# Kernel tuning notes

Hardware: AMD Instinct MI355X
Metric: run time of the kernel (lower is better)

Reference implementation:

```python
import jax, jax.numpy as jnp
import numpy as np

E = 8          # num_experts
K = 2          # top_k
CAPF = 1.25    # capacity_factor
DIM = 512
HID = 2048     # int(dim * mlp_ratio)


def setup_inputs() -> dict:
    key = jax.random.key(0)
    ks = jax.random.split(key, 5)
    s = 0.02
    x = jax.random.normal(ks[0], (8, 2048, DIM), jnp.float32)
    Wr = jax.random.normal(ks[1], (E, DIM), jnp.float32) * s          # router weight (no bias)
    W1 = jax.random.normal(ks[2], (E, HID, DIM), jnp.float32) * s     # fc1 weights per expert
    b1 = jnp.zeros((E, HID), jnp.float32)
    W2 = jax.random.normal(ks[3], (E, DIM, HID), jnp.float32) * s     # fc2 weights per expert
    b2 = jnp.zeros((E, DIM), jnp.float32)
    return {"x": x, "Wr": Wr, "W1": W1, "b1": b1, "W2": W2, "b2": b2}


def _capacity_keep(top_w, top_idx, cap):
    """For each (slot, expert), keep only the `cap` highest-weight tokens.
    top_w, top_idx: [T, K]. Returns bool keep mask [T, K]."""
    def per_slot(w, idx):
        order = jnp.argsort(-w)                       # tokens sorted by weight desc
        idx_sorted = idx[order]                       # [T] expert id in sorted order
        oh = jax.nn.one_hot(idx_sorted, E, dtype=jnp.int32)
        rank = jnp.cumsum(oh, axis=0) - 1             # rank within each expert
        r = jnp.take_along_axis(rank, idx_sorted[:, None], axis=1)[:, 0]
        keep_sorted = r < cap
        return jnp.zeros(w.shape[0], bool).at[order].set(keep_sorted)
    return jax.vmap(per_slot, in_axes=(1, 1), out_axes=1)(top_w, top_idx)


def reference(x, Wr, W1, b1, W2, b2):
    b, n, d = x.shape
    T = b * n
    flat = x.reshape(T, d)

    # Router: softmax in fp32 then cast back
    logits = flat @ Wr.T                                            # [T, E]
    probs = jax.nn.softmax(logits.astype(jnp.float32), axis=-1).astype(flat.dtype)
    top_w, top_idx = jax.lax.top_k(probs, K)                        # [T, K]
    top_w = top_w / (jnp.sum(top_w, axis=-1, keepdims=True) + 1e-8)

    # Capacity-limited drop, then renormalize
    cap = max(1, int(CAPF * T * K / E))
    keep = _capacity_keep(top_w, top_idx, cap)
    top_w = jnp.where(keep, top_w, 0.0)
    top_w = top_w / jnp.clip(jnp.sum(top_w, axis=-1, keepdims=True), 1e-8, None)

    # Combine weight per (token, expert): scatter-add top_w into dense [T, E]
    rows = jnp.arange(T)[:, None]
    w_te = jnp.zeros((T, E), flat.dtype).at[rows, top_idx].add(top_w)

    # Per-expert MLP, weighted combine (w_te is 0 for unassigned/dropped pairs)
    out = jnp.zeros_like(flat)
    for e in range(E):
        h = jax.nn.gelu(flat @ W1[e].T + b1[e], approximate=False)  # [T, HID]
        y = h @ W2[e].T + b2[e]                                     # [T, D]
        out = out + w_te[:, e:e + 1] * y

    # Load-balancing aux loss
    load = jnp.sum(w_te, axis=0) / T
    importance = probs.mean(0)
    aux = jnp.sum(importance * load * float(E))
    return out.reshape(b, n, d), aux
```

## Files before the change

### kernel.cpp

```cpp
#include <hip/hip_runtime.h>
#include <hip/hip_bf16.h>
#include <math.h>

#define DIM 512
#define HID 2048
#define NE  8
#define CSTRIDE 32

typedef __attribute__((ext_vector_type(8))) short short8;
typedef __attribute__((ext_vector_type(4))) float f32x4;
typedef unsigned short ushort_t;

static __device__ __forceinline__ ushort_t f2bf(float f) {
    unsigned int x = __builtin_bit_cast(unsigned int, f);
    unsigned int lsb = (x >> 16) & 1u;
    x += 0x7fffu + lsb;
    return (ushort_t)(x >> 16);
}
static __device__ __forceinline__ float bf2f(ushort_t u) {
    unsigned int x = ((unsigned int)u) << 16;
    return __builtin_bit_cast(float, x);
}

static __device__ __forceinline__ float fast_gelu(float v) {
    float u = v * 0.70710678118654752f;
    float s = fabsf(u);
    float t = __builtin_amdgcn_rcpf(1.f + 0.3275911f * s);
    float poly = ((((1.061405429f * t - 1.453152027f) * t + 1.421413741f) * t
                   - 0.284496736f) * t + 0.254829592f) * t;
    float e = __expf(-s * s);
    float erfv = copysignf(1.f - poly * e, u);
    return 0.5f * v * (1.f + erfv);
}

static __device__ __forceinline__ void gld16(const void* g, void* l) {
    __builtin_amdgcn_global_load_lds(
        (const __attribute__((address_space(1))) void*)g,
        (__attribute__((address_space(3))) void*)l,
        16, 0, 0);
}

__global__ void k_cvt(const float* __restrict__ src, ushort_t* __restrict__ dst, int n) {
    int i = blockIdx.x * blockDim.x + threadIdx.x;
    int stride = gridDim.x * blockDim.x;
    int n4 = n >> 2;
    for (int j = i; j < n4; j += stride) {
        float4 v = ((const float4*)src)[j];
        ushort4 o;
        o.x = f2bf(v.x); o.y = f2bf(v.y); o.z = f2bf(v.z); o.w = f2bf(v.w);
        ((ushort4*)dst)[j] = o;
    }
}

__global__ __launch_bounds__(256) void k_router(const float* __restrict__ x,
    const float* __restrict__ Wr, ushort_t* __restrict__ xb,
    float* __restrict__ probs, int* __restrict__ tidx, float* __restrict__ tw, int T)
{
    int lane = threadIdx.x & 63;
    int t = blockIdx.x * 4 + (threadIdx.x >> 6);
    if (t >= T) return;
    const float* xr = x + (size_t)t * DIM;
    double acc[NE];
#pragma unroll
    for (int e = 0; e < NE; e++) acc[e] = 0.0;
    for (int i = lane; i < DIM; i += 64) {
        float xv = xr[i];
        xb[(size_t)t * DIM + i] = f2bf(xv);
        double xd = (double)xv;
#pragma unroll
        for (int e = 0; e < NE; e++) acc[e] += xd * (double)Wr[e * DIM + i];
    }
#pragma unroll
    for (int e = 0; e < NE; e++) {
#pragma unroll
        for (int off = 32; off > 0; off >>= 1) acc[e] += __shfl_xor(acc[e], off);
    }
    double mx = acc[0];
#pragma unroll
    for (int e = 1; e < NE; e++) mx = fmax(mx, acc[e]);
    double p[NE], sum = 0.0;
#pragma unroll
    for (int e = 0; e < NE; e++) { p[e] = exp(acc[e] - mx); sum += p[e]; }
    float pr[NE];
#pragma unroll
    for (int e = 0; e < NE; e++) pr[e] = (float)(p[e] / sum);
    if (lane < NE) probs[(size_t)t * NE + lane] = pr[lane];
    if (lane == 0) {
        int i1 = 0; float b1v = pr[0];
#pragma unroll
        for (int e = 1; e < NE; e++) if (pr[e] > b1v) { b1v = pr[e]; i1 = e; }
        int i2 = -1; float b2v = -1.f;
#pragma unroll
        for (int e = 0; e < NE; e++) if (e != i1 && pr[e] > b2v) { b2v = pr[e]; i2 = e; }
        float s2 = b1v + b2v + 1e-8f;
        tidx[t * 2] = i1; tidx[t * 2 + 1] = i2;
        tw[t * 2] = b1v / s2; tw[t * 2 + 1] = b2v / s2;
    }
}

__global__ __launch_bounds__(256) void k_hist(const int* __restrict__ tidx,
                                              int* __restrict__ cnt, int T) {
    __shared__ int h[16];
    if (threadIdx.x < 16) h[threadIdx.x] = 0;
    __syncthreads();
    int stride = gridDim.x * blockDim.x;
    for (int t = blockIdx.x * blockDim.x + threadIdx.x; t < T; t += stride) {
        atomicAdd(&h[tidx[t * 2]], 1);
        atomicAdd(&h[8 + tidx[t * 2 + 1]], 1);
    }
    __syncthreads();
    if (threadIdx.x < 16 && h[threadIdx.x] != 0)
        atomicAdd(&cnt[threadIdx.x * CSTRIDE], h[threadIdx.x]);
}

__global__ void k_keep(const int* __restrict__ tidx, const float* __restrict__ tw,
                       const int* __restrict__ cnt, float* __restrict__ tw2, int T, int cap)
{
    int t = blockIdx.x * blockDim.x + threadIdx.x;
    if (t >= T) return;
    float wk[2];
#pragma unroll
    for (int s = 0; s < 2; s++) {
        int e = tidx[t * 2 + s];
        float w = tw[t * 2 + s];
        wk[s] = w;
        if (cnt[(s * NE + e) * CSTRIDE] > cap) {
            int rank = 0;
            for (int t2 = 0; t2 < T; t2++) {
                if (tidx[t2 * 2 + s] == e) {
                    float w2 = tw[t2 * 2 + s];
                    if (w2 > w || (w2 == w && t2 < t)) rank++;
                }
            }
            if (rank >= cap) wk[s] = 0.f;
        }
    }
    float denom = fmaxf(wk[0] + wk[1], 1e-8f);
    tw2[t * 2]     = wk[0] / denom;
    tw2[t * 2 + 1] = wk[1] / denom;
}

__global__ __launch_bounds__(256) void k_build(const int* __restrict__ tidx,
        const float* __restrict__ tw2, int* __restrict__ lcnt,
        int* __restrict__ ltok, int* __restrict__ pos, int T, int capM)
{
    __shared__ int h[NE];
    __shared__ int base[NE];
    if (threadIdx.x < NE) h[threadIdx.x] = 0;
    __syncthreads();
    int t = blockIdx.x * blockDim.x + threadIdx.x;
    int myE[2] = {-1, -1};
    int myp[2] = {0, 0};
    if (t < T) {
#pragma unroll
        for (int s = 0; s < 2; s++) {
            float w = tw2[t * 2 + s];
            if (w != 0.f) {
                int e = tidx[t * 2 + s];
                myE[s] = e;
                myp[s] = atomicAdd(&h[e], 1);
            }
        }
    }
    __syncthreads();
    if (threadIdx.x < NE)
        base[threadIdx.x] = (h[threadIdx.x] != 0)
            ? atomicAdd(&lcnt[threadIdx.x * CSTRIDE], h[threadIdx.x]) : 0;
    __syncthreads();
    if (t < T) {
#pragma unroll
        for (int s = 0; s < 2; s++) {
            if (myE[s] >= 0) {
                int p = base[myE[s]] + myp[s];
                ltok[myE[s] * capM + p] = t;
                pos[t * 2 + s] = (myE[s] << 20) | p;
            } else {
                pos[t * 2 + s] = -1;
            }
        }
    }
}

__global__ void k_off(const int* __restrict__ lcnt, int* __restrict__ loff) {
    if (threadIdx.x == 0 && blockIdx.x == 0) {
        int o = 0;
        for (int e = 0; e < NE; e++) {
            loff[e] = o;
            o += ((lcnt[e * CSTRIDE] + 127) >> 7) << 7;
        }
        loff[NE] = o;
    }
}

__global__ __launch_bounds__(256) void k_fc1(
    const ushort_t* __restrict__ xb, const ushort_t* __restrict__ W1b,
    const float* __restrict__ b1, const int* __restrict__ lcnt,
    const int* __restrict__ loff, const int* __restrict__ ltok,
    ushort_t* __restrict__ hbuf, int capM)
{
    int bx = blockIdx.x;
    int e  = bx & 7;
    int r  = bx >> 3;
    int mt = r >> 4;
    int nt = r & 15;
    int cnt = lcnt[e * CSTRIDE];
    if (cnt > capM) cnt = capM;
    int m0 = mt * 128;
    if (m0 >= cnt) return;
    int n0 = nt * 128;
    const int* toks = ltok + e * capM;
    int hrow0 = loff[e] + m0;
    const ushort_t* Bsrc = W1b + (size_t)e * HID * DIM;

    __shared__ char smem[65536];
    char* As0 = smem;          char* Bs0 = smem + 16384;
    char* As1 = smem + 32768;  char* Bs1 = smem + 49152;

    int tid = threadIdx.x;
    int wave = tid >> 6, lane = tid & 63;
    int wm = wave >> 1, wn = wave & 1;

    const char* aSrc[4]; const char* bSrc[4]; int ldst[4];
#pragma unroll
    for (int i = 0; i < 4; i++) {
        int c = tid + 256 * i;
        int row = c >> 3, cc = c & 7;
        int scc = cc ^ (row & 7);
        int gr = m0 + row;
        int tok = toks[gr < cnt ? gr : (cnt - 1)];
        aSrc[i] = (const char*)(xb + (size_t)tok * DIM + scc * 8);
        bSrc[i] = (const char*)(Bsrc + (size_t)(n0 + row) * DIM + scc * 8);
        ldst[i] = (i * 256 + wave * 64) * 16;
    }

    f32x4 acc[4][4];
#pragma unroll
    for (int a = 0; a < 4; a++)
#pragma unroll
        for (int b = 0; b < 4; b++) acc[a][b] = (f32x4){0.f, 0.f, 0.f, 0.f};

    int aRow = wm * 64 + (lane & 15);
    int bRow = wn * 64 + (lane & 15);
    int kq = lane >> 4;

    auto STAGE = [&](int kt, char* A, char* B) {
#pragma unroll
        for (int i = 0; i < 4; i++) {
            gld16(aSrc[i] + kt * 128, A + ldst[i]);
            gld16(bSrc[i] + kt * 128, B + ldst[i]);
        }
    };
    auto COMPUTE = [&](const char* A, const char* B) {
#pragma unroll
        for (int kk = 0; kk < 2; kk++) {
            int c16 = kk * 4 + kq;
            short8 af[4], bfr[4];
#pragma unroll
            for (int mf = 0; mf < 4; mf++) {
                int rr = aRow + mf * 16;
                af[mf] = *(const short8*)(A + rr * 128 + ((c16 ^ (rr & 7)) << 4));
            }
#pragma unroll
            for (int nf = 0; nf < 4; nf++) {
                int rr = bRow + nf * 16;
                bfr[nf] = *(const short8*)(B + rr * 128 + ((c16 ^ (rr & 7)) << 4));
            }
#pragma unroll
            for (int mf = 0; mf < 4; mf++)
#pragma unroll
                for (int nf = 0; nf < 4; nf++)
                    acc[mf][nf] = __builtin_amdgcn_mfma_f32_16x16x32_bf16(bfr[nf], af[mf], acc[mf][nf], 0, 0, 0);
        }
    };

    const int NT = DIM / 64;
    char *Ac = As0, *Bc = Bs0, *An = As1, *Bn = Bs1;
    STAGE(0, Ac, Bc);
    __syncthreads();
    for (int kt = 0; kt < NT; kt++) {
        if (kt + 1 < NT) STAGE(kt + 1, An, Bn);
        COMPUTE(Ac, Bc);
        __syncthreads();
        char* t0 = Ac; Ac = An; An = t0;
        char* t1 = Bc; Bc = Bn; Bn = t1;
    }

    const float* b1e = b1 + e * HID;
    int mlocal = wm * 64 + (lane & 15);
    int nbase0 = n0 + wn * 64 + (lane >> 4) * 4;
#pragma unroll
    for (int mf = 0; mf < 4; mf++) {
        int mrow = mlocal + mf * 16;
        bool valid = (m0 + mrow) < cnt;
        ushort_t* dst = hbuf + (size_t)(hrow0 + mrow) * HID;
#pragma unroll
        for (int nf = 0; nf < 4; nf++) {
            int nc = nbase0 + nf * 16;
            float4 bias4 = *(const float4*)(b1e + nc);
            ushort4 o;
            o.x = f2bf(fast_gelu(acc[mf][nf][0] + bias4.x));
            o.y = f2bf(fast_gelu(acc[mf][nf][1] + bias4.y));
            o.z = f2bf(fast_gelu(acc[mf][nf][2] + bias4.z));
            o.w = f2bf(fast_gelu(acc[mf][nf][3] + bias4.w));
            if (valid) *(ushort4*)(dst + nc) = o;
        }
    }
}

__global__ __launch_bounds__(256) void k_fc2(
    const ushort_t* __restrict__ hbuf, const ushort_t* __restrict__ W2b,
    const float* __restrict__ b2, const int* __restrict__ lcnt,
    const int* __restrict__ loff, ushort_t* __restrict__ ybuf, int capM)
{
    int bx = blockIdx.x;
    int e  = bx & 7;
    int r  = bx >> 3;
    int mt = r >> 2;
    int nt = r & 3;
    int cnt = lcnt[e * CSTRIDE];
    if (cnt > capM) cnt = capM;
    int m0 = mt * 128;
    if (m0 >= cnt) return;
    int n0 = nt * 128;
    int hrow0 = loff[e] + m0;
    const ushort_t* Bsrc = W2b + (size_t)e * DIM * HID;

    __shared__ char smem[65536];
    char* As0 = smem;          char* Bs0 = smem + 16384;
    char* As1 = smem + 32768;  char* Bs1 = smem + 49152;

    int tid = threadIdx.x;
    int wave = tid >> 6, lane = tid & 63;
    int wm = wave >> 1, wn = wave & 1;

    const char* aSrc[4]; const char* bSrc[4]; int ldst[4];
#pragma unroll
    for (int i = 0; i < 4; i++) {
        int c = tid + 256 * i;
        int row = c >> 3, cc = c & 7;
        int scc = cc ^ (row & 7);
        aSrc[i] = (const char*)(hbuf + (size_t)(hrow0 + row) * HID + scc * 8);
        bSrc[i] = (const char*)(Bsrc + (size_t)(n0 + row) * HID + scc * 8);
        ldst[i] = (i * 256 + wave * 64) * 16;
    }

    f32x4 acc[4][4];
#pragma unroll
    for (int a = 0; a < 4; a++)
#pragma unroll
        for (int b = 0; b < 4; b++) acc[a][b] = (f32x4){0.f, 0.f, 0.f, 0.f};

    int aRow = wm * 64 + (lane & 15);
    int bRow = wn * 64 + (lane & 15);
    int kq = lane >> 4;

    auto STAGE = [&](int kt, char* A, char* B) {
#pragma unroll
        for (int i = 0; i < 4; i++) {
            gld16(aSrc[i] + kt * 128, A + ldst[i]);
            gld16(bSrc[i] + kt * 128, B + ldst[i]);
        }
    };
    auto COMPUTE = [&](const char* A, const char* B) {
#pragma unroll
        for (int kk = 0; kk < 2; kk++) {
            int c16 = kk * 4 + kq;
            short8 af[4], bfr[4];
#pragma unroll
            for (int mf = 0; mf < 4; mf++) {
                int rr = aRow + mf * 16;
                af[mf] = *(const short8*)(A + rr * 128 + ((c16 ^ (rr & 7)) << 4));
            }
#pragma unroll
            for (int nf = 0; nf < 4; nf++) {
                int rr = bRow + nf * 16;
                bfr[nf] = *(const short8*)(B + rr * 128 + ((c16 ^ (rr & 7)) << 4));
            }
#pragma unroll
            for (int mf = 0; mf < 4; mf++)
#pragma unroll
                for (int nf = 0; nf < 4; nf++)
                    acc[mf][nf] = __builtin_amdgcn_mfma_f32_16x16x32_bf16(bfr[nf], af[mf], acc[mf][nf], 0, 0, 0);
        }
    };

    const int NT = HID / 64;
    char *Ac = As0, *Bc = Bs0, *An = As1, *Bn = Bs1;
    STAGE(0, Ac, Bc);
    __syncthreads();
    for (int kt = 0; kt < NT; kt++) {
        if (kt + 1 < NT) STAGE(kt + 1, An, Bn);
        COMPUTE(Ac, Bc);
        __syncthreads();
        char* t0 = Ac; Ac = An; An = t0;
        char* t1 = Bc; Bc = Bn; Bn = t1;
    }

    const float* b2e = b2 + e * DIM;
    int mlocal = wm * 64 + (lane & 15);
    int nbase0 = n0 + wn * 64 + (lane >> 4) * 4;
#pragma unroll
    for (int mf = 0; mf < 4; mf++) {
        int mrow = mlocal + mf * 16;
        bool valid = (m0 + mrow) < cnt;
        ushort_t* dst = ybuf + (size_t)(hrow0 + mrow) * DIM;
#pragma unroll
        for (int nf = 0; nf < 4; nf++) {
            int nc = nbase0 + nf * 16;
            float4 bias4 = *(const float4*)(b2e + nc);
            ushort4 o;
            o.x = f2bf(acc[mf][nf][0] + bias4.x);
            o.y = f2bf(acc[mf][nf][1] + bias4.y);
            o.z = f2bf(acc[mf][nf][2] + bias4.z);
            o.w = f2bf(acc[mf][nf][3] + bias4.w);
            if (valid) *(ushort4*)(dst + nc) = o;
        }
    }
}

__global__ __launch_bounds__(256) void k_comb(const ushort_t* __restrict__ ybuf,
    const float* __restrict__ tw2, const int* __restrict__ pos,
    const int* __restrict__ loff, float* __restrict__ out, int T, int capM)
{
    int wv = threadIdx.x >> 6, lane = threadIdx.x & 63;
    int t = blockIdx.x * 4 + wv;
    if (t >= T) return;
    float o[8];
#pragma unroll
    for (int j = 0; j < 8; j++) o[j] = 0.f;
#pragma unroll
    for (int s = 0; s < 2; s++) {
        int pk = pos[t * 2 + s];
        if (pk >= 0) {
            float w = tw2[t * 2 + s];
            int e = pk >> 20, p = pk & 0xFFFFF;
            int row = loff[e] + p;
            short8 y = *(const short8*)(ybuf + (size_t)row * DIM + lane * 8);
#pragma unroll
            for (int j = 0; j < 8; j++) o[j] += w * bf2f((ushort_t)y[j]);
        }
    }
    float4* dst = (float4*)(out + (size_t)t * DIM + lane * 8);
    dst[0] = (float4){o[0], o[1], o[2], o[3]};
    dst[1] = (float4){o[4], o[5], o[6], o[7]};
}

__global__ __launch_bounds__(256) void k_aux1(const float* __restrict__ probs,
    const float* __restrict__ tw2, const int* __restrict__ tidx,
    float* __restrict__ partial, int T)
{
    __shared__ float red[256 * 16];
    float imp[NE], ld[NE];
#pragma unroll
    for (int e = 0; e < NE; e++) { imp[e] = 0.f; ld[e] = 0.f; }
    int stride = gridDim.x * blockDim.x;
    for (int t = blockIdx.x * blockDim.x + threadIdx.x; t < T; t += stride) {
#pragma unroll
        for (int e = 0; e < NE; e++) imp[e] += probs[(size_t)t * NE + e];
#pragma unroll
        for (int s = 0; s < 2; s++) ld[tidx[t * 2 + s]] += tw2[t * 2 + s];
    }
#pragma unroll
    for (int e = 0; e < NE; e++) {
        red[threadIdx.x * 16 + e] = imp[e];
        red[threadIdx.x * 16 + 8 + e] = ld[e];
    }
    __syncthreads();
    for (int off = 128; off > 0; off >>= 1) {
        if (threadIdx.x < off) {
#pragma unroll
            for (int j = 0; j < 16; j++)
                red[threadIdx.x * 16 + j] += red[(threadIdx.x + off) * 16 + j];
        }
        __syncthreads();
    }
    if (threadIdx.x < 16) partial[blockIdx.x * 16 + threadIdx.x] = red[threadIdx.x];
}

__global__ void k_aux2(const float* __restrict__ partial, float* __restrict__ outaux,
                       int nb, int T)
{
    __shared__ float s[16];
    if (threadIdx.x < 16) {
        float a = 0.f;
        for (int b = 0; b < nb; b++) a += partial[b * 16 + threadIdx.x];
        s[threadIdx.x] = a;
    }
    __syncthreads();
    if (threadIdx.x == 0) {
        float invT = 1.f / (float)T;
        float aux = 0.f;
        for (int e = 0; e < NE; e++)
            aux += (s[e] * invT) * (s[8 + e] * invT) * (float)NE;
        outaux[0] = aux;
    }
}

extern "C" void kernel_launch(void* const* d_in, const int* in_sizes, int n_in,
                              void* d_out, int out_size, void* d_ws, size_t ws_size,
                              hipStream_t stream)
{
    const float* x  = (const float*)d_in[0];
    const float* Wr = (const float*)d_in[1];
    const float* W1 = (const float*)d_in[2];
    const float* b1 = (const float*)d_in[3];
    const float* W2 = (const float*)d_in[4];
    const float* b2 = (const float*)d_in[5];
    float* out = (float*)d_out;

    int T = in_sizes[0] / DIM;
    int cap = (int)(1.25 * (double)T * 2.0 / 8.0);
    if (cap < 1) cap = 1;
    int capM = 2 * cap; if (capM > T) capM = T;
    int mtmax = (capM + 127) / 128;

    char* w = (char*)d_ws;
    size_t off = 0;
    auto alloc = [&](size_t bytes) {
        char* p = w + off;
        off = (off + bytes + 255) & ~(size_t)255;
        return p;
    };
    size_t ybrows = (size_t)T * 2 + NE * 128;
    size_t ybbytes = ybrows * DIM * 2;
    ushort_t* ybuf = (ushort_t*)w;
    ushort_t* xb   = (ushort_t*)alloc((size_t)T * DIM * 2);
    ushort_t* W1b  = (ushort_t*)alloc((size_t)NE * HID * DIM * 2);
    if (off < ybbytes) off = (ybbytes + 255) & ~(size_t)255;
    ushort_t* W2b  = (ushort_t*)alloc((size_t)NE * DIM * HID * 2);
    ushort_t* hbuf = (ushort_t*)alloc(ybrows * HID * 2);
    float* probs   = (float*)alloc((size_t)T * NE * 4);
    int*   tidx    = (int*)alloc((size_t)T * 2 * 4);
    float* tw      = (float*)alloc((size_t)T * 2 * 4);
    float* tw2     = (float*)alloc((size_t)T * 2 * 4);
    int*   pos     = (int*)alloc((size_t)T * 2 * 4);
    int*   cnt     = (int*)alloc(16 * CSTRIDE * 4);
    int*   lcnt    = (int*)alloc(NE * CSTRIDE * 4);
    int*   loff    = (int*)alloc((NE + 1) * 4);
    int*   ltok    = (int*)alloc((size_t)NE * capM * 4);
    float* partial = (float*)alloc(64 * 16 * 4);

    (void)hipMemsetAsync(cnt, 0, 16 * CSTRIDE * 4, stream);
    (void)hipMemsetAsync(lcnt, 0, NE * CSTRIDE * 4, stream);

    k_cvt<<<2048, 256, 0, stream>>>(W1, W1b, NE * HID * DIM);
    k_cvt<<<2048, 256, 0, stream>>>(W2, W2b, NE * DIM * HID);
    k_router<<<(T + 3) / 4, 256, 0, stream>>>(x, Wr, xb, probs, tidx, tw, T);
    k_hist<<<64, 256, 0, stream>>>(tidx, cnt, T);
    k_keep<<<(T + 255) / 256, 256, 0, stream>>>(tidx, tw, cnt, tw2, T, cap);
    k_build<<<(T + 255) / 256, 256, 0, stream>>>(tidx, tw2, lcnt, ltok, pos, T, capM);
    k_off<<<1, 64, 0, stream>>>(lcnt, loff);

    k_fc1<<<NE * mtmax * (HID / 128), 256, 0, stream>>>(
        xb, W1b, b1, lcnt, loff, ltok, hbuf, capM);
    k_fc2<<<NE * mtmax * (DIM / 128), 256, 0, stream>>>(
        hbuf, W2b, b2, lcnt, loff, ybuf, capM);
    k_comb<<<(T + 3) / 4, 256, 0, stream>>>(ybuf, tw2, pos, loff, out, T, capM);

    k_aux1<<<64, 256, 0, stream>>>(probs, tw2, tidx, partial, T);
    k_aux2<<<1, 64, 0, stream>>>(partial, out + (size_t)T * DIM, 64, T);
}
```

Before: 306.6 us.

## Single-buffer LDS in expert GEMMs to raise occupancy, precompute swizzled offsets

Both expert GEMM kernels (fc1, fc2) move from a double-buffered 64KB LDS tile to a single 32KB buffer with load→sync→compute→sync per K step, and declare launch bounds of 4 blocks per CU. The aim is more resident blocks per CU so that other blocks hide the global-load latency that the in-block prefetch used to cover. LDS read offsets with the XOR swizzle are precomputed once per thread, and the K loop is unrolled with fixed immediate offsets to cut address arithmetic. In exchange, each block now stalls on every tile load with no intra-block overlap and adds a second barrier per step. The register cap implied by the occupancy hint may also cause spills.

```diff
diff --git a/kernel.cpp b/kernel.cpp
--- a/kernel.cpp
+++ b/kernel.cpp
@@ -192,7 +192,7 @@
     }
 }
 
-__global__ __launch_bounds__(256) void k_fc1(
+__global__ __launch_bounds__(256, 4) void k_fc1(
     const ushort_t* __restrict__ xb, const ushort_t* __restrict__ W1b,
     const float* __restrict__ b1, const int* __restrict__ lcnt,
     const int* __restrict__ loff, const int* __restrict__ ltok,
@@ -212,9 +212,9 @@
     int hrow0 = loff[e] + m0;
     const ushort_t* Bsrc = W1b + (size_t)e * HID * DIM;
 
-    __shared__ char smem[65536];
-    char* As0 = smem;          char* Bs0 = smem + 16384;
-    char* As1 = smem + 32768;  char* Bs1 = smem + 49152;
+    __shared__ char smem[32768];
+    char* As = smem;
+    char* Bs = smem + 16384;
 
     int tid = threadIdx.x;
     int wave = tid >> 6, lane = tid & 63;
@@ -242,29 +242,28 @@
     int aRow = wm * 64 + (lane & 15);
     int bRow = wn * 64 + (lane & 15);
     int kq = lane >> 4;
-
-    auto STAGE = [&](int kt, char* A, char* B) {
+    int swz0 = (kq ^ (lane & 7)) << 4;
+    int swz1 = ((4 + kq) ^ (lane & 7)) << 4;
+    int aoff[2] = { aRow * 128 + swz0, aRow * 128 + swz1 };
+    int boff[2] = { bRow * 128 + swz0, bRow * 128 + swz1 };
+
+    auto STAGE = [&](int kofs) {
 #pragma unroll
         for (int i = 0; i < 4; i++) {
-            gld16(aSrc[i] + kt * 128, A + ldst[i]);
-            gld16(bSrc[i] + kt * 128, B + ldst[i]);
+            gld16(aSrc[i] + kofs, As + ldst[i]);
+            gld16(bSrc[i] + kofs, Bs + ldst[i]);
         }
     };
-    auto COMPUTE = [&](const char* A, const char* B) {
+    auto COMPUTE = [&]() {
 #pragma unroll
         for (int kk = 0; kk < 2; kk++) {
-            int c16 = kk * 4 + kq;
             short8 af[4], bfr[4];
 #pragma unroll
-            for (int mf = 0; mf < 4; mf++) {
-                int rr = aRow + mf * 16;
-                af[mf] = *(const short8*)(A + rr * 128 + ((c16 ^ (rr & 7)) << 4));
-            }
-#pragma unroll
-            for (int nf = 0; nf < 4; nf++) {
-                int rr = bRow + nf * 16;
-                bfr[nf] = *(const short8*)(B + rr * 128 + ((c16 ^ (rr & 7)) << 4));
-            }
+            for (int mf = 0; mf < 4; mf++)
+                af[mf] = *(const short8*)(As + aoff[kk] + mf * 2048);
+#pragma unroll
+            for (int nf = 0; nf < 4; nf++)
+                bfr[nf] = *(const short8*)(Bs + boff[kk] + nf * 2048);
 #pragma unroll
             for (int mf = 0; mf < 4; mf++)
 #pragma unroll
@@ -273,16 +272,12 @@
         }
     };
 
-    const int NT = DIM / 64;
-    char *Ac = As0, *Bc = Bs0, *An = As1, *Bn = Bs1;
-    STAGE(0, Ac, Bc);
-    __syncthreads();
-    for (int kt = 0; kt < NT; kt++) {
-        if (kt + 1 < NT) STAGE(kt + 1, An, Bn);
-        COMPUTE(Ac, Bc);
+#pragma unroll
+    for (int kt = 0; kt < DIM / 64; kt++) {
+        STAGE(kt * 128);
         __syncthreads();
-        char* t0 = Ac; Ac = An; An = t0;
-        char* t1 = Bc; Bc = Bn; Bn = t1;
+        COMPUTE();
+        __syncthreads();
     }
 
     const float* b1e = b1 + e * HID;
@@ -307,7 +302,7 @@
     }
 }
 
-__global__ __launch_bounds__(256) void k_fc2(
+__global__ __launch_bounds__(256, 4) void k_fc2(
     const ushort_t* __restrict__ hbuf, const ushort_t* __restrict__ W2b,
     const float* __restrict__ b2, const int* __restrict__ lcnt,
     const int* __restrict__ loff, ushort_t* __restrict__ ybuf, int capM)
@@ -325,9 +320,9 @@
     int hrow0 = loff[e] + m0;
     const ushort_t* Bsrc = W2b + (size_t)e * DIM * HID;
 
-    __shared__ char smem[65536];
-    char* As0 = smem;          char* Bs0 = smem + 16384;
-    char* As1 = smem + 32768;  char* Bs1 = smem + 49152;
+    __shared__ char smem[32768];
+    char* As = smem;
+    char* Bs = smem + 16384;
 
     int tid = threadIdx.x;
     int wave = tid >> 6, lane = tid & 63;
@@ -353,29 +348,28 @@
     int aRow = wm * 64 + (lane & 15);
     int bRow = wn * 64 + (lane & 15);
     int kq = lane >> 4;
-
-    auto STAGE = [&](int kt, char* A, char* B) {
+    int swz0 = (kq ^ (lane & 7)) << 4;
+    int swz1 = ((4 + kq) ^ (lane & 7)) << 4;
+    int aoff[2] = { aRow * 128 + swz0, aRow * 128 + swz1 };
+    int boff[2] = { bRow * 128 + swz0, bRow * 128 + swz1 };
+
+    auto STAGE = [&](int kofs) {
 #pragma unroll
         for (int i = 0; i < 4; i++) {
-            gld16(aSrc[i] + kt * 128, A + ldst[i]);
-            gld16(bSrc[i] + kt * 128, B + ldst[i]);
+            gld16(aSrc[i] + kofs, As + ldst[i]);
+            gld16(bSrc[i] + kofs, Bs + ldst[i]);
         }
     };
-    auto COMPUTE = [&](const char* A, const char* B) {
+    auto COMPUTE = [&]() {
 #pragma unroll
         for (int kk = 0; kk < 2; kk++) {
-            int c16 = kk * 4 + kq;
             short8 af[4], bfr[4];
 #pragma unroll
-            for (int mf = 0; mf < 4; mf++) {
-                int rr = aRow + mf * 16;
-                af[mf] = *(const short8*)(A + rr * 128 + ((c16 ^ (rr & 7)) << 4));
-            }
-#pragma unroll
-            for (int nf = 0; nf < 4; nf++) {
-                int rr = bRow + nf * 16;
-                bfr[nf] = *(const short8*)(B + rr * 128 + ((c16 ^ (rr & 7)) << 4));
-            }
+            for (int mf = 0; mf < 4; mf++)
+                af[mf] = *(const short8*)(As + aoff[kk] + mf * 2048);
+#pragma unroll
+            for (int nf = 0; nf < 4; nf++)
+                bfr[nf] = *(const short8*)(Bs + boff[kk] + nf * 2048);
 #pragma unroll
             for (int mf = 0; mf < 4; mf++)
 #pragma unroll
@@ -384,16 +378,16 @@
         }
     };
 
-    const int NT = HID / 64;
-    char *Ac = As0, *Bc = Bs0, *An = As1, *Bn = Bs1;
-    STAGE(0, Ac, Bc);
-    __syncthreads();
-    for (int kt = 0; kt < NT; kt++) {
-        if (kt + 1 < NT) STAGE(kt + 1, An, Bn);
-        COMPUTE(Ac, Bc);
-        __syncthreads();
-        char* t0 = Ac; Ac = An; An = t0;
-        char* t1 = Bc; Bc = Bn; Bn = t1;
+    for (int kg = 0; kg < 4; kg++) {
+#pragma unroll
+        for (int k8 = 0; k8 < 8; k8++) {
+            STAGE(k8 * 128);
+            __syncthreads();
+            COMPUTE();
+            __syncthreads();
+        }
+#pragma unroll
+        for (int i = 0; i < 4; i++) { aSrc[i] += 1024; bSrc[i] += 1024; }
     }
 
     const float* b2e = b2 + e * DIM;
```

Result: no change. 301.0 us (-1.8%).
